# Optimization experiments

Hardware: AMD Instinct MI355X
Metric: run time of the kernel (lower is better)

The kernel has to match this reference:

```python
import jax, jax.numpy as jnp
import numpy as np

HID = 1024
HEADS = 16
HEAD_DIM = HID // HEADS
MAX_P = 64
TAB = 2 * MAX_P + 1
B, L = 8, 512


def setup_inputs() -> dict:
    key = jax.random.key(0)
    ks = jax.random.split(key, 16)
    def lin(k, fan_in, fan_out):
        lim = 1.0 / np.sqrt(fan_in)
        kw, kb = jax.random.split(k)
        W = jax.random.uniform(kw, (fan_out, fan_in), jnp.float32, -lim, lim)
        b = jax.random.uniform(kb, (fan_out,), jnp.float32, -lim, lim)
        return W, b
    Wq, bq = lin(ks[0], HID, HID)
    Wk, bk = lin(ks[1], HID, HID)
    Wv, bv = lin(ks[2], HID, HID)
    Wo, bo = lin(ks[3], HID, HID)
    # xavier_uniform for relative-position tables
    xlim = float(np.sqrt(6.0 / (TAB + HEAD_DIM)))
    table_k = jax.random.uniform(ks[4], (TAB, HEAD_DIM), jnp.float32, -xlim, xlim)
    table_v = jax.random.uniform(ks[5], (TAB, HEAD_DIM), jnp.float32, -xlim, xlim)
    return {
        "query": jax.random.normal(ks[6], (B, L, HID), jnp.float32),
        "key": jax.random.normal(ks[7], (B, L, HID), jnp.float32),
        "value": jax.random.normal(ks[8], (B, L, HID), jnp.float32),
        "final_mat": jax.random.randint(ks[9], (B, L, L), 0, TAB, jnp.int64 if jax.config.jax_enable_x64 else jnp.int32),
        "Wq": Wq, "bq": bq, "Wk": Wk, "bk": bk,
        "Wv": Wv, "bv": bv, "Wo": Wo, "bo": bo,
        "table_k": table_k, "table_v": table_v,
    }


def reference(query, key, value, final_mat, Wq, bq, Wk, bk, Wv, bv, Wo, bo, table_k, table_v):
    Bt, Lq, D = query.shape
    H, hd = HEADS, HEAD_DIM
    q = query @ Wq.T + bq          # [B,Lq,D]
    k = key @ Wk.T + bk            # [B,Lk,D]
    v = value @ Wv.T + bv          # [B,Lv,D]
    q4 = q.reshape(Bt, Lq, H, hd)
    k4 = k.reshape(Bt, -1, H, hd)
    v4 = v.reshape(Bt, -1, H, hd)
    # content-content scores
    attn1 = jnp.einsum('bqhd,bkhd->bhqk', q4, k4)
    # content-position scores via gathered relative-key embeddings [B,Lq,Lk,hd]
    rk = table_k[final_mat]
    attn2 = jnp.einsum('bqhd,bqkd->bhqk', q4, rk)
    scale = jnp.asarray(np.sqrt(hd), q.dtype)
    attn = jax.nn.softmax((attn1 + attn2) / scale, axis=-1)  # [B,H,Lq,Lk]
    # dropout p=0 (eval)
    w1 = jnp.einsum('bhqk,bkhd->bqhd', attn, v4)
    rv = table_v[final_mat]                                   # [B,Lq,Lk,hd]
    w2 = jnp.einsum('bhqk,bqkd->bqhd', attn, rv)
    x = (w1 + w2).reshape(Bt, Lq, D)
    return x @ Wo.T + bo
```

## Files before the change

### kernel.cpp

```cpp
#include <hip/hip_runtime.h>

#define HID 1024
#define HEADS 16
#define HD 64
#define TAB 129
#define QSTR 136
#define BATCH 8
#define SEQ 512

typedef unsigned int uint;
typedef unsigned short ushort;
typedef unsigned char uchar;
typedef __attribute__((ext_vector_type(4))) float f32x4;
typedef __attribute__((ext_vector_type(8))) __bf16 bf16x8;

__device__ __forceinline__ ushort f2b(float x) {
    uint b = __float_as_uint(x);
    uint r = (b + 0x7fffu + ((b >> 16) & 1u)) >> 16;
    return (ushort)r;
}
__device__ __forceinline__ uint pk(float lo, float hi) {
    return (uint)f2b(lo) | ((uint)f2b(hi) << 16);
}
__device__ __forceinline__ float b2f(ushort u) {
    return __uint_as_float(((uint)u) << 16);
}
union U16x8 { uint u[4]; bf16x8 v; ushort s[8]; uint4 q; };
__device__ __forceinline__ bf16x8 pack8(float a0, float a1, float a2, float a3,
                                        float a4, float a5, float a6, float a7) {
    U16x8 r;
    r.u[0] = pk(a0, a1); r.u[1] = pk(a2, a3);
    r.u[2] = pk(a4, a5); r.u[3] = pk(a6, a7);
    return r.v;
}

__device__ __forceinline__ void keep(bf16x8& v) {
    uint4* u = (uint4*)&v;
    asm volatile("" : "+v"(u->x), "+v"(u->y), "+v"(u->z), "+v"(u->w));
}
__device__ __forceinline__ void keepu(uint& v) {
    asm volatile("" : "+v"(v));
}

#define GL16(gp, lp) __builtin_amdgcn_global_load_lds( \
    (const __attribute__((address_space(1))) void*)(gp), \
    (__attribute__((address_space(3))) void*)(lp), 16, 0, 0)

#define LDS_BARRIER() do { \
        asm volatile("s_waitcnt lgkmcnt(0)" ::: "memory"); \
        __builtin_amdgcn_s_barrier(); \
    } while (0)

struct ConvArgs { const float* src[7]; ushort* dst[7]; };

__global__ __launch_bounds__(256) void convert_bf16(ConvArgs ca) {
    int bid = blockIdx.x;
    int ti, lb;
    if (bid < 6144) { ti = bid >> 11; lb = bid & 2047; }
    else { int r = bid - 6144; ti = 3 + (r >> 9); lb = r & 511; }
    const float* s = ca.src[ti] + (size_t)lb * 2048 + (threadIdx.x << 3);
    ushort*      d = ca.dst[ti] + (size_t)lb * 2048 + (threadIdx.x << 3);
    float4 a = *(const float4*)s;
    float4 c = *(const float4*)(s + 4);
    uint4 u;
    u.x = pk(a.x, a.y); u.y = pk(a.z, a.w);
    u.z = pk(c.x, c.y); u.w = pk(c.z, c.w);
    *(uint4*)d = u;
}

struct GemmArgs {
    const ushort* A[3];
    const ushort* W[3];
    const float*  bias[3];
    float*        Cf[3];
    ushort*       Cb[3];
};

__global__ __launch_bounds__(256) void gemm_bf16(GemmArgs ga, int M, int N, int K) {
    __shared__ ushort As[2][128 * 32];
    __shared__ ushort Bs[2][128 * 32];
    const int z = blockIdx.z;
    const ushort* A = ga.A[z];
    const ushort* W = ga.W[z];
    const int tid = threadIdx.x;
    const int m0 = blockIdx.y * 128;
    const int n0 = blockIdx.x * 128;

    const int w  = tid >> 6;
    const int l  = tid & 63;
    const int lr = l & 15;
    const int lg = l >> 4;
    const int wm = w >> 1;
    const int wn = w & 1;

    const int sr = tid >> 2;
    const int sc = tid & 3;
    const int g  = sc ^ ((sr >> 1) & 3);
    const ushort* Ag0 = A + (size_t)(m0 + sr)      * K + g * 8;
    const ushort* Ag1 = A + (size_t)(m0 + sr + 64) * K + g * 8;
    const ushort* Wg0 = W + (size_t)(n0 + sr)      * K + g * 8;
    const ushort* Wg1 = W + (size_t)(n0 + sr + 64) * K + g * 8;

    f32x4 acc[4][4];
#pragma unroll
    for (int mt = 0; mt < 4; ++mt)
#pragma unroll
        for (int nt = 0; nt < 4; ++nt) acc[mt][nt] = (f32x4){0.f, 0.f, 0.f, 0.f};

#define STAGE(buf, k0) do { \
        GL16(Ag0 + (k0), &As[buf][w * 512]); \
        GL16(Ag1 + (k0), &As[buf][2048 + w * 512]); \
        GL16(Wg0 + (k0), &Bs[buf][w * 512]); \
        GL16(Wg1 + (k0), &Bs[buf][2048 + w * 512]); \
    } while (0)

    const int swz = (lr >> 1) & 3;
#define COMPUTE(buf) do { \
        bf16x8 af[4], bf[4]; \
        _Pragma("unroll") \
        for (int mt = 0; mt < 4; ++mt) \
            af[mt] = *(const bf16x8*)&As[buf][(wm * 64 + mt * 16 + lr) * 32 + (lg ^ swz) * 8]; \
        _Pragma("unroll") \
        for (int nt = 0; nt < 4; ++nt) \
            bf[nt] = *(const bf16x8*)&Bs[buf][(wn * 64 + nt * 16 + lr) * 32 + (lg ^ swz) * 8]; \
        _Pragma("unroll") \
        for (int mt = 0; mt < 4; ++mt) \
            _Pragma("unroll") \
            for (int nt = 0; nt < 4; ++nt) \
                acc[mt][nt] = __builtin_amdgcn_mfma_f32_16x16x32_bf16(af[mt], bf[nt], acc[mt][nt], 0, 0, 0); \
    } while (0)

    STAGE(0, 0);
    __syncthreads();
    const int nk = K / 32;
    for (int t = 0; t < nk - 1; ++t) {
        STAGE((t + 1) & 1, (size_t)(t + 1) * 32);
        COMPUTE(t & 1);
        __syncthreads();
    }
    COMPUTE((nk - 1) & 1);

    const float* bias = ga.bias[z];
    float bv[4];
#pragma unroll
    for (int nt = 0; nt < 4; ++nt) bv[nt] = bias[n0 + wn * 64 + nt * 16 + lr];
    float*  Cf = ga.Cf[z];
    ushort* Cb = ga.Cb[z];
    if (Cf) {
#pragma unroll
        for (int mt = 0; mt < 4; ++mt)
#pragma unroll
            for (int r4 = 0; r4 < 4; ++r4) {
                size_t m = m0 + wm * 64 + mt * 16 + lg * 4 + r4;
                float* crow = Cf + m * N + n0 + wn * 64 + lr;
#pragma unroll
                for (int nt = 0; nt < 4; ++nt)
                    crow[nt * 16] = acc[mt][nt][r4] + bv[nt];
            }
    } else {
#pragma unroll
        for (int mt = 0; mt < 4; ++mt)
#pragma unroll
            for (int r4 = 0; r4 < 4; ++r4) {
                size_t m = m0 + wm * 64 + mt * 16 + lg * 4 + r4;
                ushort* crow = Cb + m * N + n0 + wn * 64 + lr;
#pragma unroll
                for (int nt = 0; nt < 4; ++nt)
                    crow[nt * 16] = f2b(acc[mt][nt][r4] + bv[nt]);
            }
    }
#undef STAGE
#undef COMPUTE
}

__global__ __launch_bounds__(256) void gemm_wo(const ushort* __restrict__ A,
                                               const ushort* __restrict__ W,
                                               const float* __restrict__ bias,
                                               float* __restrict__ Cf) {
    const int M = BATCH * SEQ, N = HID, K = HID;
    __shared__ ushort As[2][128 * 32];
    __shared__ ushort Bs[2][64 * 32];
    const int tid = threadIdx.x;
    const int m0 = blockIdx.y * 128;
    const int n0 = blockIdx.x * 64;

    const int w  = tid >> 6;
    const int l  = tid & 63;
    const int lr = l & 15;
    const int lg = l >> 4;
    const int wm = w >> 1;
    const int wn = w & 1;

    const int sr = tid >> 2;
    const int sc = tid & 3;
    const int g  = sc ^ ((sr >> 1) & 3);
    const ushort* Ag0 = A + (size_t)(m0 + sr)      * K + g * 8;
    const ushort* Ag1 = A + (size_t)(m0 + sr + 64) * K + g * 8;
    const ushort* Wg0 = W + (size_t)(n0 + sr)      * K + g * 8;

    f32x4 acc[4][2];
#pragma unroll
    for (int mt = 0; mt < 4; ++mt)
#pragma unroll
        for (int nt = 0; nt < 2; ++nt) acc[mt][nt] = (f32x4){0.f, 0.f, 0.f, 0.f};

#define STAGE(buf, k0) do { \
        GL16(Ag0 + (k0), &As[buf][w * 512]); \
        GL16(Ag1 + (k0), &As[buf][2048 + w * 512]); \
        GL16(Wg0 + (k0), &Bs[buf][w * 512]); \
    } while (0)

    const int swz = (lr >> 1) & 3;
#define COMPUTE(buf) do { \
        bf16x8 af[4], bf[2]; \
        _Pragma("unroll") \
        for (int mt = 0; mt < 4; ++mt) \
            af[mt] = *(const bf16x8*)&As[buf][(wm * 64 + mt * 16 + lr) * 32 + (lg ^ swz) * 8]; \
        _Pragma("unroll") \
        for (int nt = 0; nt < 2; ++nt) \
            bf[nt] = *(const bf16x8*)&Bs[buf][(wn * 32 + nt * 16 + lr) * 32 + (lg ^ swz) * 8]; \
        _Pragma("unroll") \
        for (int mt = 0; mt < 4; ++mt) \
            _Pragma("unroll") \
            for (int nt = 0; nt < 2; ++nt) \
                acc[mt][nt] = __builtin_amdgcn_mfma_f32_16x16x32_bf16(af[mt], bf[nt], acc[mt][nt], 0, 0, 0); \
    } while (0)

    STAGE(0, 0);
    __syncthreads();
    const int nk = K / 32;
    for (int t = 0; t < nk - 1; ++t) {
        STAGE((t + 1) & 1, (size_t)(t + 1) * 32);
        COMPUTE(t & 1);
        __syncthreads();
    }
    COMPUTE((nk - 1) & 1);

    float bv[2];
#pragma unroll
    for (int nt = 0; nt < 2; ++nt) bv[nt] = bias[n0 + wn * 32 + nt * 16 + lr];
#pragma unroll
    for (int mt = 0; mt < 4; ++mt)
#pragma unroll
        for (int r4 = 0; r4 < 4; ++r4) {
            size_t m = m0 + wm * 64 + mt * 16 + lg * 4 + r4;
            float* crow = Cf + m * N + n0 + wn * 32 + lr;
#pragma unroll
            for (int nt = 0; nt < 2; ++nt)
                crow[nt * 16] = acc[mt][nt][r4] + bv[nt];
        }
#undef STAGE
#undef COMPUTE
}

__global__ __launch_bounds__(256) void prep_kernel(const ushort* __restrict__ qb,
                                                   const float* __restrict__ table_k,
                                                   const ushort* __restrict__ vb,
                                                   const float* __restrict__ table_v,
                                                   const int* __restrict__ fmat,
                                                   ushort* __restrict__ qtab,
                                                   ushort* __restrict__ vT,
                                                   ushort* __restrict__ tvT,
                                                   uchar* __restrict__ fm8) {
    __shared__ __align__(16) ushort shmem[144 * 72];
    const int wg  = blockIdx.x;
    const int tid = threadIdx.x;

    if (wg < 256) {
        const int h    = wg & 15;
        const int half = (wg >> 4) & 1;
        const int b    = wg >> 5;
        const int q0   = half * 256;
        ushort* tk = shmem;
        for (int i = tid; i < TAB * 8; i += 256) {
            int row = i >> 3, gr = i & 7;
            const float* src = table_k + row * HD + gr * 8;
            float4 a = *(const float4*)src;
            float4 c = *(const float4*)(src + 4);
            uint4 u;
            u.x = pk(a.x, a.y); u.y = pk(a.z, a.w);
            u.z = pk(c.x, c.y); u.w = pk(c.z, c.w);
            *(uint4*)&tk[row * 72 + gr * 8] = u;
        }
        __syncthreads();

        const int w  = tid >> 6;
        const int l  = tid & 63;
        const int lr = l & 15;
        const int lg = l >> 4;
        bf16x8 qf[4][2];
#pragma unroll
        for (int qt = 0; qt < 4; ++qt) {
            const ushort* qrow = qb + ((size_t)(b * SEQ) + q0 + w * 64 + qt * 16 + lr) * HID + h * HD;
            qf[qt][0] = *(const bf16x8*)(qrow + lg * 8);
            qf[qt][1] = *(const bf16x8*)(qrow + 32 + lg * 8);
        }
        ushort* outbase = qtab + ((size_t)(b * HEADS + h) * SEQ + q0 + w * 64) * QSTR;
#pragma unroll
        for (int mt = 0; mt < 9; ++mt) {
            bf16x8 tf0 = *(const bf16x8*)&tk[(mt * 16 + lr) * 72 + lg * 8];
            bf16x8 tf1 = *(const bf16x8*)&tk[(mt * 16 + lr) * 72 + 32 + lg * 8];
#pragma unroll
            for (int qt = 0; qt < 4; ++qt) {
                f32x4 acc = (f32x4){0.f, 0.f, 0.f, 0.f};
                acc = __builtin_amdgcn_mfma_f32_16x16x32_bf16(tf0, qf[qt][0], acc, 0, 0, 0);
                acc = __builtin_amdgcn_mfma_f32_16x16x32_bf16(tf1, qf[qt][1], acc, 0, 0, 0);
                ushort* orow = outbase + (size_t)(qt * 16 + lr) * QSTR;
                if (mt < 8) {
                    uint2 pu;
                    pu.x = pk(acc[0], acc[1]); pu.y = pk(acc[2], acc[3]);
                    *(uint2*)&orow[mt * 16 + lg * 4] = pu;
                } else if (lg == 0) {
                    orow[128] = f2b(acc[0]);
                }
            }
        }
    } else if (wg < 768) {
        const int vw = wg - 256;
        ushort* tile = shmem;
        const int b = vw >> 6, h = (vw >> 2) & 15, kc = vw & 3;
        const int k0 = kc * 128;
        {
            const int kr = tid >> 1, dc = (tid & 1) * 32;
            const ushort* src = vb + ((size_t)(b * SEQ) + k0 + kr) * HID + h * 64 + dc;
#pragma unroll
            for (int j = 0; j < 4; ++j) {
                uint4 u = *(const uint4*)(src + j * 8);
                *(uint4*)&tile[kr * 72 + dc + j * 8] = u;
            }
        }
        __syncthreads();
        {
            const int dr = tid >> 2, kc2 = (tid & 3) * 32;
            ushort* dst = vT + ((size_t)(b * 16 + h) * 64 + dr) * 512 + k0 + kc2;
#pragma unroll
            for (int j = 0; j < 4; ++j) {
                U16x8 o;
#pragma unroll
                for (int i = 0; i < 8; ++i)
                    o.s[i] = tile[(kc2 + j * 8 + i) * 72 + dr];
                *(uint4*)(dst + j * 8) = o.q;
            }
        }
    } else if (wg == 768) {
        const int tt = tid >> 1, dc = (tid & 1) * 32;
        const float* src = table_v + (size_t)tt * HD + dc;
#pragma unroll
        for (int i = 0; i < 32; ++i)
            tvT[(size_t)(dc + i) * 128 + tt] = f2b(src[i]);
    } else {
        const size_t base = (size_t)(wg - 769) * 2048 + (size_t)tid * 8;
        int4 a = *(const int4*)(fmat + base);
        int4 c = *(const int4*)(fmat + base + 4);
        uint lo = (uint)a.x | ((uint)a.y << 8) | ((uint)a.z << 16) | ((uint)a.w << 24);
        uint hi = (uint)c.x | ((uint)c.y << 8) | ((uint)c.z << 16) | ((uint)c.w << 24);
        uint2 o; o.x = lo; o.y = hi;
        *(uint2*)(fm8 + base) = o;
    }
}

__global__ __launch_bounds__(256, 3) void attn_mfma(const ushort* __restrict__ qp,
                                                    const ushort* __restrict__ kp,
                                                    const ushort* __restrict__ vT,
                                                    const ushort* __restrict__ qt,
                                                    const uchar* __restrict__ fm8,
                                                    const float* __restrict__ table_v,
                                                    const ushort* __restrict__ tvT,
                                                    ushort* __restrict__ x) {
    constexpr float FIX = 65536.0f;
    constexpr float INV_FIX = 1.0f / 65536.0f;

    __shared__ __align__(16) ushort qtb[16 * QSTR];
    __shared__ __align__(16) uint   sbin[16 * 132];
    __shared__ __align__(16) ushort P[4][16 * 136];
    __shared__ float rowsumw[4][16];

    const int tid = threadIdx.x;
    const int w   = tid >> 6;
    const int l   = tid & 63;
    const int lr  = l & 15;
    const int lg  = l >> 4;

    const int wg   = blockIdx.x;
    const int work = (wg & 7) * 512 + (wg >> 3);
    const int qblk = work & 31;
    const int h    = (work >> 5) & 15;
    const int b    = work >> 9;
    const int q0   = qblk * 16;
    const size_t bSEQ = (size_t)b * SEQ;
    const int hHD = h * HD;

    const uchar*  fmrow8   = fm8 + (bSEQ + q0 + lr) * SEQ;
    const ushort* kfr_base = kp + (bSEQ + lr) * HID + hHD;
    const ushort* vfr_base = vT + ((size_t)(b * HEADS + h) * HD + lr) * SEQ;

    bf16x8 qfrag[2];
    {
        const ushort* qrow = qp + (bSEQ + q0 + lr) * HID + hHD;
        qfrag[0] = *(const bf16x8*)(qrow + lg * 8);
        qfrag[1] = *(const bf16x8*)(qrow + 32 + lg * 8);
    }

    {
        const uint4* src = (const uint4*)(qt + ((size_t)(b * HEADS + h) * SEQ + q0) * QSTR);
        uint4* dst = (uint4*)qtb;
        for (int i = tid; i < 16 * QSTR / 8; i += 256) dst[i] = src[i];
    }
    {
        uint4 z = {0u, 0u, 0u, 0u};
        uint4* dz = (uint4*)sbin;
        for (int i = tid; i < 16 * 132 / 4; i += 256) dz[i] = z;
    }
    LDS_BARRIER();

    bf16x8 kfr[8][2];
    uint   fmu[8];
#pragma unroll
    for (int i = 0; i < 8; ++i) {
        const int t  = i >> 2;
        const int mt = i & 3;
        const int k0 = (w * 2 + t) * 64;
        const ushort* kr = kfr_base + (size_t)(k0 + mt * 16) * HID;
        kfr[i][0] = *(const bf16x8*)(kr + lg * 8);
        kfr[i][1] = *(const bf16x8*)(kr + 32 + lg * 8);
        fmu[i] = *(const uint*)(fmrow8 + k0 + mt * 16 + lg * 4);
    }
#pragma unroll
    for (int i = 0; i < 8; ++i) { keep(kfr[i][0]); keep(kfr[i][1]); keepu(fmu[i]); }

    f32x4 stv[8];
#pragma unroll
    for (int i = 0; i < 8; ++i) {
        f32x4 st = (f32x4){0.f, 0.f, 0.f, 0.f};
        st = __builtin_amdgcn_mfma_f32_16x16x32_bf16(kfr[i][0], qfrag[0], st, 0, 0, 0);
        st = __builtin_amdgcn_mfma_f32_16x16x32_bf16(kfr[i][1], qfrag[1], st, 0, 0, 0);
        stv[i] = st;
    }

    float lsum = 0.f;
#pragma unroll
    for (int i = 0; i < 8; ++i) {
        const int t  = i >> 2;
        const int mt = i & 3;
        const uint fm = fmu[i];
        const int t0 = fm & 255, t1 = (fm >> 8) & 255, t2 = (fm >> 16) & 255, t3 = fm >> 24;
        const f32x4 st = stv[i];
        float pr0 = __expf((st[0] + b2f(qtb[lr * QSTR + t0])) * 0.125f);
        float pr1 = __expf((st[1] + b2f(qtb[lr * QSTR + t1])) * 0.125f);
        float pr2 = __expf((st[2] + b2f(qtb[lr * QSTR + t2])) * 0.125f);
        float pr3 = __expf((st[3] + b2f(qtb[lr * QSTR + t3])) * 0.125f);
        lsum += pr0 + pr1 + pr2 + pr3;
        __hip_atomic_fetch_add(&sbin[lr * 132 + t0], (uint)(pr0 * FIX),
                               __ATOMIC_RELAXED, __HIP_MEMORY_SCOPE_WORKGROUP);
        __hip_atomic_fetch_add(&sbin[lr * 132 + t1], (uint)(pr1 * FIX),
                               __ATOMIC_RELAXED, __HIP_MEMORY_SCOPE_WORKGROUP);
        __hip_atomic_fetch_add(&sbin[lr * 132 + t2], (uint)(pr2 * FIX),
                               __ATOMIC_RELAXED, __HIP_MEMORY_SCOPE_WORKGROUP);
        __hip_atomic_fetch_add(&sbin[lr * 132 + t3], (uint)(pr3 * FIX),
                               __ATOMIC_RELAXED, __HIP_MEMORY_SCOPE_WORKGROUP);
        uint2 pu;
        pu.x = pk(pr0, pr1); pu.y = pk(pr2, pr3);
        *(uint2*)&P[w][lr * 136 + t * 64 + mt * 16 + lg * 4] = pu;
    }
    lsum += __shfl_xor(lsum, 16);
    lsum += __shfl_xor(lsum, 32);
    if (lg == 0) rowsumw[w][lr] = lsum;

    bf16x8 vfr[2][4][2];
#pragma unroll
    for (int t = 0; t < 2; ++t) {
        const int k0 = (w * 2 + t) * 64;
#pragma unroll
        for (int nt = 0; nt < 4; ++nt) {
            const ushort* vr = vfr_base + (size_t)nt * 16 * SEQ + k0;
            vfr[t][nt][0] = *(const bf16x8*)(vr + lg * 8);
            vfr[t][nt][1] = *(const bf16x8*)(vr + 32 + lg * 8);
        }
    }
#pragma unroll
    for (int t = 0; t < 2; ++t)
#pragma unroll
        for (int nt = 0; nt < 4; ++nt) { keep(vfr[t][nt][0]); keep(vfr[t][nt][1]); }

    f32x4 acc_o[4];
#pragma unroll
    for (int nt = 0; nt < 4; ++nt) acc_o[nt] = (f32x4){0.f, 0.f, 0.f, 0.f};
#pragma unroll
    for (int t = 0; t < 2; ++t) {
        bf16x8 pa0 = *(const bf16x8*)&P[w][lr * 136 + t * 64 + lg * 8];
        bf16x8 pa1 = *(const bf16x8*)&P[w][lr * 136 + t * 64 + 32 + lg * 8];
#pragma unroll
        for (int nt = 0; nt < 4; ++nt) {
            acc_o[nt] = __builtin_amdgcn_mfma_f32_16x16x32_bf16(pa0, vfr[t][nt][0], acc_o[nt], 0, 0, 0);
            acc_o[nt] = __builtin_amdgcn_mfma_f32_16x16x32_bf16(pa1, vfr[t][nt][1], acc_o[nt], 0, 0, 0);
        }
    }

    LDS_BARRIER();

    {
        const uint* sp = &sbin[lr * 132 + w * 32 + lg * 8];
        bf16x8 af = pack8((float)sp[0] * INV_FIX, (float)sp[1] * INV_FIX,
                          (float)sp[2] * INV_FIX, (float)sp[3] * INV_FIX,
                          (float)sp[4] * INV_FIX, (float)sp[5] * INV_FIX,
                          (float)sp[6] * INV_FIX, (float)sp[7] * INV_FIX);
#pragma unroll
        for (int nt = 0; nt < 4; ++nt) {
            bf16x8 bf_ = *(const bf16x8*)(tvT + (size_t)(nt * 16 + lr) * 128 + w * 32 + lg * 8);
            acc_o[nt] = __builtin_amdgcn_mfma_f32_16x16x32_bf16(af, bf_, acc_o[nt], 0, 0, 0);
        }
    }

    float* obuf = (float*)&P[0][0];
    if (w != 0) {
#pragma unroll
        for (int nt = 0; nt < 4; ++nt)
            *(f32x4*)&obuf[(((w - 1) * 4 + nt) * 64 + l) * 4] = acc_o[nt];
    }
    LDS_BARRIER();

    if (w == 0) {
#pragma unroll
        for (int j = 0; j < 3; ++j)
#pragma unroll
            for (int nt = 0; nt < 4; ++nt) {
                f32x4 p_ = *(const f32x4*)&obuf[((j * 4 + nt) * 64 + l) * 4];
                acc_o[nt][0] += p_[0]; acc_o[nt][1] += p_[1];
                acc_o[nt][2] += p_[2]; acc_o[nt][3] += p_[3];
            }
        float iv[4], nb[4];
#pragma unroll
        for (int r = 0; r < 4; ++r) {
            const int q = lg * 4 + r;
            iv[r] = 1.f / (rowsumw[0][q] + rowsumw[1][q] + rowsumw[2][q] + rowsumw[3][q]);
            nb[r] = (float)sbin[q * 132 + 128] * INV_FIX;
        }
        ushort* orow = x + (bSEQ + q0 + lg * 4) * HID + hHD;
#pragma unroll
        for (int nt = 0; nt < 4; ++nt) {
            float tv = table_v[(size_t)128 * HD + nt * 16 + lr];
#pragma unroll
            for (int r = 0; r < 4; ++r) {
                float o = (acc_o[nt][r] + nb[r] * tv) * iv[r];
                orow[(size_t)r * HID + nt * 16 + lr] = f2b(o);
            }
        }
    }
}

extern "C" void kernel_launch(void* const* d_in, const int* in_sizes, int n_in,
                              void* d_out, int out_size, void* d_ws, size_t ws_size,
                              hipStream_t stream) {
    const float* query = (const float*)d_in[0];
    const float* key   = (const float*)d_in[1];
    const float* value = (const float*)d_in[2];
    const int*   fmat  = (const int*)d_in[3];
    const float* Wq = (const float*)d_in[4];
    const float* bq = (const float*)d_in[5];
    const float* Wk = (const float*)d_in[6];
    const float* bk = (const float*)d_in[7];
    const float* Wv = (const float*)d_in[8];
    const float* bv = (const float*)d_in[9];
    const float* Wo = (const float*)d_in[10];
    const float* bo = (const float*)d_in[11];
    const float* table_k = (const float*)d_in[12];
    const float* table_v = (const float*)d_in[13];

    const size_t nBLD = (size_t)BATCH * SEQ * HID;
    const size_t nW   = (size_t)HID * HID;
    ushort* us = (ushort*)d_ws;
    ushort* qin16 = us;                 us += nBLD;
    ushort* kin16 = us;                 us += nBLD;
    ushort* vin16 = us;                 us += nBLD;
    ushort* wq16  = us;                 us += nW;
    ushort* wk16  = us;                 us += nW;
    ushort* wv16  = us;                 us += nW;
    ushort* wo16  = us;                 us += nW;
    ushort* qb16  = us;                 us += nBLD;
    ushort* kb16  = us;                 us += nBLD;
    ushort* vb16  = us;                 us += nBLD;
    ushort* qt16  = us;                 us += (size_t)BATCH * HEADS * SEQ * QSTR;
    ushort* xb16  = us;                 us += nBLD;
    uchar*  fm8   = (uchar*)us;

    ConvArgs ca;
    ca.src[0] = query; ca.src[1] = key; ca.src[2] = value;
    ca.src[3] = Wq; ca.src[4] = Wk; ca.src[5] = Wv; ca.src[6] = Wo;
    ca.dst[0] = qin16; ca.dst[1] = kin16; ca.dst[2] = vin16;
    ca.dst[3] = wq16; ca.dst[4] = wk16; ca.dst[5] = wv16; ca.dst[6] = wo16;
    convert_bf16<<<dim3(8192), 256, 0, stream>>>(ca);

    const int M = BATCH * SEQ;

    GemmArgs gq = {};
    gq.A[0] = qin16; gq.A[1] = kin16; gq.A[2] = vin16;
    gq.W[0] = wq16;  gq.W[1] = wk16;  gq.W[2] = wv16;
    gq.bias[0] = bq; gq.bias[1] = bk; gq.bias[2] = bv;
    gq.Cf[0] = nullptr; gq.Cf[1] = nullptr; gq.Cf[2] = nullptr;
    gq.Cb[0] = qb16; gq.Cb[1] = kb16; gq.Cb[2] = vb16;
    gemm_bf16<<<dim3(HID / 128, M / 128, 3), 256, 0, stream>>>(gq, M, HID, HID);

    ushort* vTbuf  = qin16;
    ushort* tvTbuf = kin16;

    prep_kernel<<<dim3(1793), 256, 0, stream>>>(qb16, table_k, vb16, table_v,
                                                fmat, qt16, vTbuf, tvTbuf, fm8);

    attn_mfma<<<dim3(BATCH * HEADS * (SEQ/16)), 256, 0, stream>>>(
        qb16, kb16, vTbuf, qt16, fm8, table_v, tvTbuf, xb16);

    gemm_wo<<<dim3(HID / 64, M / 128), 256, 0, stream>>>(xb16, wo16, bo, (float*)d_out);
}
```

Baseline: 198.6 us.

## Split fused attention into separate QK GEMM, softmax and PV GEMM kernels

```diff
diff --git a/kernel.cpp b/kernel.cpp
--- a/kernel.cpp
+++ b/kernel.cpp
@@ -26,30 +26,10 @@
     return __uint_as_float(((uint)u) << 16);
 }
 union U16x8 { uint u[4]; bf16x8 v; ushort s[8]; uint4 q; };
-__device__ __forceinline__ bf16x8 pack8(float a0, float a1, float a2, float a3,
-                                        float a4, float a5, float a6, float a7) {
-    U16x8 r;
-    r.u[0] = pk(a0, a1); r.u[1] = pk(a2, a3);
-    r.u[2] = pk(a4, a5); r.u[3] = pk(a6, a7);
-    return r.v;
-}
-
-__device__ __forceinline__ void keep(bf16x8& v) {
-    uint4* u = (uint4*)&v;
-    asm volatile("" : "+v"(u->x), "+v"(u->y), "+v"(u->z), "+v"(u->w));
-}
-__device__ __forceinline__ void keepu(uint& v) {
-    asm volatile("" : "+v"(v));
-}
 
 #define GL16(gp, lp) __builtin_amdgcn_global_load_lds( \
     (const __attribute__((address_space(1))) void*)(gp), \
     (__attribute__((address_space(3))) void*)(lp), 16, 0, 0)
-
-#define LDS_BARRIER() do { \
-        asm volatile("s_waitcnt lgkmcnt(0)" ::: "memory"); \
-        __builtin_amdgcn_s_barrier(); \
-    } while (0)
 
 struct ConvArgs { const float* src[7]; ushort* dst[7]; };
 
@@ -260,7 +240,7 @@
                                                    const int* __restrict__ fmat,
                                                    ushort* __restrict__ qtab,
                                                    ushort* __restrict__ vT,
-                                                   ushort* __restrict__ tvT,
+                                                   ushort* __restrict__ tvT2,
                                                    uchar* __restrict__ fm8) {
     __shared__ __align__(16) ushort shmem[144 * 72];
     const int wg  = blockIdx.x;
@@ -343,11 +323,11 @@
             }
         }
     } else if (wg == 768) {
-        const int tt = tid >> 1, dc = (tid & 1) * 32;
-        const float* src = table_v + (size_t)tt * HD + dc;
-#pragma unroll
-        for (int i = 0; i < 32; ++i)
-            tvT[(size_t)(dc + i) * 128 + tt] = f2b(src[i]);
+        for (int i = tid; i < 64 * 160; i += 256) {
+            int d = i / 160;
+            int c = i - d * 160;
+            tvT2[i] = (c < TAB) ? f2b(table_v[(size_t)c * HD + d]) : (ushort)0;
+        }
     } else {
         const size_t base = (size_t)(wg - 769) * 2048 + (size_t)tid * 8;
         int4 a = *(const int4*)(fmat + base);
@@ -359,193 +339,226 @@
     }
 }
 
-__global__ __launch_bounds__(256, 3) void attn_mfma(const ushort* __restrict__ qp,
-                                                    const ushort* __restrict__ kp,
-                                                    const ushort* __restrict__ vT,
-                                                    const ushort* __restrict__ qt,
-                                                    const uchar* __restrict__ fm8,
-                                                    const float* __restrict__ table_v,
-                                                    const ushort* __restrict__ tvT,
-                                                    ushort* __restrict__ x) {
+__global__ __launch_bounds__(256) void qk_gemm(const ushort* __restrict__ qb,
+                                               const ushort* __restrict__ kb,
+                                               ushort* __restrict__ S) {
+    __shared__ ushort As[2][128 * 32];
+    __shared__ ushort Bs[2][128 * 32];
+    const int tid = threadIdx.x;
+    const int m0 = blockIdx.x * 128;
+    const int n0 = blockIdx.y * 128;
+    const int bh = blockIdx.z;
+    const int b = bh >> 4, h = bh & 15;
+    const size_t rowQ = (size_t)b * SEQ;
+
+    const int w  = tid >> 6;
+    const int l  = tid & 63;
+    const int lr = l & 15;
+    const int lg = l >> 4;
+    const int wm = w >> 1;
+    const int wn = w & 1;
+
+    const int sr = tid >> 2;
+    const int sc = tid & 3;
+    const int g  = sc ^ ((sr >> 1) & 3);
+    const ushort* Ag0 = qb + (rowQ + m0 + sr)      * HID + h * HD + g * 8;
+    const ushort* Ag1 = qb + (rowQ + m0 + sr + 64) * HID + h * HD + g * 8;
+    const ushort* Wg0 = kb + (rowQ + n0 + sr)      * HID + h * HD + g * 8;
+    const ushort* Wg1 = kb + (rowQ + n0 + sr + 64) * HID + h * HD + g * 8;
+
+    GL16(Ag0,      &As[0][w * 512]); GL16(Ag1,      &As[0][2048 + w * 512]);
+    GL16(Wg0,      &Bs[0][w * 512]); GL16(Wg1,      &Bs[0][2048 + w * 512]);
+    GL16(Ag0 + 32, &As[1][w * 512]); GL16(Ag1 + 32, &As[1][2048 + w * 512]);
+    GL16(Wg0 + 32, &Bs[1][w * 512]); GL16(Wg1 + 32, &Bs[1][2048 + w * 512]);
+
+    f32x4 acc[4][4];
+#pragma unroll
+    for (int mt = 0; mt < 4; ++mt)
+#pragma unroll
+        for (int nt = 0; nt < 4; ++nt) acc[mt][nt] = (f32x4){0.f, 0.f, 0.f, 0.f};
+
+    const int swz = (lr >> 1) & 3;
+    __syncthreads();
+#pragma unroll
+    for (int buf = 0; buf < 2; ++buf) {
+        bf16x8 af[4], bf[4];
+#pragma unroll
+        for (int mt = 0; mt < 4; ++mt)
+            af[mt] = *(const bf16x8*)&As[buf][(wm * 64 + mt * 16 + lr) * 32 + (lg ^ swz) * 8];
+#pragma unroll
+        for (int nt = 0; nt < 4; ++nt)
+            bf[nt] = *(const bf16x8*)&Bs[buf][(wn * 64 + nt * 16 + lr) * 32 + (lg ^ swz) * 8];
+#pragma unroll
+        for (int mt = 0; mt < 4; ++mt)
+#pragma unroll
+            for (int nt = 0; nt < 4; ++nt)
+                acc[mt][nt] = __builtin_amdgcn_mfma_f32_16x16x32_bf16(af[mt], bf[nt], acc[mt][nt], 0, 0, 0);
+    }
+
+    ushort* Sb = S + (size_t)bh * SEQ * SEQ;
+#pragma unroll
+    for (int mt = 0; mt < 4; ++mt)
+#pragma unroll
+        for (int r4 = 0; r4 < 4; ++r4) {
+            int m = m0 + wm * 64 + mt * 16 + lg * 4 + r4;
+            ushort* srow = Sb + (size_t)m * SEQ + n0 + wn * 64 + lr;
+#pragma unroll
+            for (int nt = 0; nt < 4; ++nt)
+                srow[nt * 16] = f2b(acc[mt][nt][r4]);
+        }
+}
+
+__global__ __launch_bounds__(256) void sm_kernel(ushort* __restrict__ S,
+                                                 const ushort* __restrict__ qt,
+                                                 const uchar* __restrict__ fm8,
+                                                 ushort* __restrict__ binbuf) {
     constexpr float FIX = 65536.0f;
     constexpr float INV_FIX = 1.0f / 65536.0f;
-
-    __shared__ __align__(16) ushort qtb[16 * QSTR];
-    __shared__ __align__(16) uint   sbin[16 * 132];
-    __shared__ __align__(16) ushort P[4][16 * 136];
-    __shared__ float rowsumw[4][16];
-
+    __shared__ uint binsL[4][160];
     const int tid = threadIdx.x;
-    const int w   = tid >> 6;
+    const int wv  = tid >> 6;
     const int l   = tid & 63;
-    const int lr  = l & 15;
-    const int lg  = l >> 4;
-
-    const int wg   = blockIdx.x;
-    const int work = (wg & 7) * 512 + (wg >> 3);
-    const int qblk = work & 31;
-    const int h    = (work >> 5) & 15;
-    const int b    = work >> 9;
-    const int q0   = qblk * 16;
-    const size_t bSEQ = (size_t)b * SEQ;
-    const int hHD = h * HD;
-
-    const uchar*  fmrow8   = fm8 + (bSEQ + q0 + lr) * SEQ;
-    const ushort* kfr_base = kp + (bSEQ + lr) * HID + hHD;
-    const ushort* vfr_base = vT + ((size_t)(b * HEADS + h) * HD + lr) * SEQ;
-
-    bf16x8 qfrag[2];
-    {
-        const ushort* qrow = qp + (bSEQ + q0 + lr) * HID + hHD;
-        qfrag[0] = *(const bf16x8*)(qrow + lg * 8);
-        qfrag[1] = *(const bf16x8*)(qrow + 32 + lg * 8);
+    const int gr0 = blockIdx.x * 32 + wv * 8;
+
+    for (int ri = 0; ri < 8; ++ri) {
+        const int gr = gr0 + ri;
+        const int q  = gr & 511;
+        const int b  = gr >> 13;
+        binsL[wv][l] = 0u;
+        binsL[wv][l + 64] = 0u;
+        if (l < 32) binsL[wv][l + 128] = 0u;
+
+        U16x8 sv;
+        sv.q = *(const uint4*)&S[((size_t)gr << 9) + l * 8];
+        const uchar* fr = fm8 + ((((size_t)b << 9) + q) << 9) + l * 8;
+        uint f0 = *(const uint*)fr;
+        uint f1 = *(const uint*)(fr + 4);
+        const ushort* qrow = qt + (size_t)gr * QSTR;
+
+        int ts[8];
+        ts[0] = f0 & 255; ts[1] = (f0 >> 8) & 255; ts[2] = (f0 >> 16) & 255; ts[3] = f0 >> 24;
+        ts[4] = f1 & 255; ts[5] = (f1 >> 8) & 255; ts[6] = (f1 >> 16) & 255; ts[7] = f1 >> 24;
+
+        float pr[8];
+        float lsum = 0.f;
+#pragma unroll
+        for (int j = 0; j < 8; ++j) {
+            float s = b2f(sv.s[j]);
+            float gv = b2f(qrow[ts[j]]);
+            pr[j] = __expf((s + gv) * 0.125f);
+            lsum += pr[j];
+        }
+#pragma unroll
+        for (int j = 0; j < 8; ++j)
+            __hip_atomic_fetch_add(&binsL[wv][ts[j]], (uint)(pr[j] * FIX),
+                                   __ATOMIC_RELAXED, __HIP_MEMORY_SCOPE_WORKGROUP);
+#pragma unroll
+        for (int off = 32; off >= 1; off >>= 1)
+            lsum += __shfl_xor(lsum, off);
+        const float invl = 1.f / lsum;
+
+        U16x8 pv;
+#pragma unroll
+        for (int j = 0; j < 4; ++j)
+            pv.u[j] = pk(pr[2 * j] * invl, pr[2 * j + 1] * invl);
+        *(uint4*)&S[((size_t)gr << 9) + l * 8] = pv.q;
+
+        asm volatile("s_waitcnt lgkmcnt(0)" ::: "memory");
+        ushort* bb = binbuf + (size_t)gr * 160;
+        const float sc = INV_FIX * invl;
+        {
+            int c = 2 * l;
+            *(uint*)&bb[c] = pk((float)binsL[wv][c] * sc, (float)binsL[wv][c + 1] * sc);
+        }
+        if (l < 16) {
+            int c = 128 + 2 * l;
+            *(uint*)&bb[c] = pk((float)binsL[wv][c] * sc, (float)binsL[wv][c + 1] * sc);
+        }
     }
-
-    {
-        const uint4* src = (const uint4*)(qt + ((size_t)(b * HEADS + h) * SEQ + q0) * QSTR);
-        uint4* dst = (uint4*)qtb;
-        for (int i = tid; i < 16 * QSTR / 8; i += 256) dst[i] = src[i];
+}
+
+__global__ __launch_bounds__(256) void pv_gemm(const ushort* __restrict__ P,
+                                               const ushort* __restrict__ binbuf,
+                                               const ushort* __restrict__ vT,
+                                               const ushort* __restrict__ tvT2,
+                                               ushort* __restrict__ x) {
+    __shared__ ushort As[2][128 * 32];
+    __shared__ ushort Bs[2][64 * 32];
+    const int tid = threadIdx.x;
+    const int m0 = blockIdx.x * 128;
+    const int bh = blockIdx.y;
+    const int b = bh >> 4, h = bh & 15;
+
+    const int w  = tid >> 6;
+    const int l  = tid & 63;
+    const int lr = l & 15;
+    const int lg = l >> 4;
+    const int wm = w >> 1;
+    const int wn = w & 1;
+
+    const int sr = tid >> 2;
+    const int sc = tid & 3;
+    const int g  = sc ^ ((sr >> 1) & 3);
+    const ushort* AgS0 = P + ((size_t)bh * SEQ + m0 + sr)      * 512 + g * 8;
+    const ushort* AgS1 = P + ((size_t)bh * SEQ + m0 + sr + 64) * 512 + g * 8;
+    const ushort* AgB0 = binbuf + ((size_t)bh * SEQ + m0 + sr)      * 160 + g * 8;
+    const ushort* AgB1 = binbuf + ((size_t)bh * SEQ + m0 + sr + 64) * 160 + g * 8;
+    const ushort* WgV  = vT + ((size_t)bh * 64 + sr) * 512 + g * 8;
+    const ushort* WgT  = tvT2 + (size_t)sr * 160 + g * 8;
+
+#define STAGE_C(buf, st) do { \
+        const ushort* a0_ = (st) < 16 ? AgS0 + (st) * 32 : AgB0 + ((st) - 16) * 32; \
+        const ushort* a1_ = (st) < 16 ? AgS1 + (st) * 32 : AgB1 + ((st) - 16) * 32; \
+        const ushort* b0_ = (st) < 16 ? WgV  + (st) * 32 : WgT  + ((st) - 16) * 32; \
+        GL16(a0_, &As[buf][w * 512]); \
+        GL16(a1_, &As[buf][2048 + w * 512]); \
+        GL16(b0_, &Bs[buf][w * 512]); \
+    } while (0)
+
+    f32x4 acc[4][2];
+#pragma unroll
+    for (int mt = 0; mt < 4; ++mt)
+#pragma unroll
+        for (int nt = 0; nt < 2; ++nt) acc[mt][nt] = (f32x4){0.f, 0.f, 0.f, 0.f};
+
+    const int swz = (lr >> 1) & 3;
+#define COMPUTE_C(buf) do { \
+        bf16x8 af[4], bf[2]; \
+        _Pragma("unroll") \
+        for (int mt = 0; mt < 4; ++mt) \
+            af[mt] = *(const bf16x8*)&As[buf][(wm * 64 + mt * 16 + lr) * 32 + (lg ^ swz) * 8]; \
+        _Pragma("unroll") \
+        for (int nt = 0; nt < 2; ++nt) \
+            bf[nt] = *(const bf16x8*)&Bs[buf][(wn * 32 + nt * 16 + lr) * 32 + (lg ^ swz) * 8]; \
+        _Pragma("unroll") \
+        for (int mt = 0; mt < 4; ++mt) \
+            _Pragma("unroll") \
+            for (int nt = 0; nt < 2; ++nt) \
+                acc[mt][nt] = __builtin_amdgcn_mfma_f32_16x16x32_bf16(af[mt], bf[nt], acc[mt][nt], 0, 0, 0); \
+    } while (0)
+
+    STAGE_C(0, 0);
+    __syncthreads();
+    const int nk = 21;
+    for (int t = 0; t < nk - 1; ++t) {
+        STAGE_C((t + 1) & 1, t + 1);
+        COMPUTE_C(t & 1);
+        __syncthreads();
     }
-    {
-        uint4 z = {0u, 0u, 0u, 0u};
-        uint4* dz = (uint4*)sbin;
-        for (int i = tid; i < 16 * 132 / 4; i += 256) dz[i] = z;
-    }
-    LDS_BARRIER();
-
-    bf16x8 kfr[8][2];
-    uint   fmu[8];
-#pragma unroll
-    for (int i = 0; i < 8; ++i) {
-        const int t  = i >> 2;
-        const int mt = i & 3;
-        const int k0 = (w * 2 + t) * 64;
-        const ushort* kr = kfr_base + (size_t)(k0 + mt * 16) * HID;
-        kfr[i][0] = *(const bf16x8*)(kr + lg * 8);
-        kfr[i][1] = *(const bf16x8*)(kr + 32 + lg * 8);
-        fmu[i] = *(const uint*)(fmrow8 + k0 + mt * 16 + lg * 4);
-    }
-#pragma unroll
-    for (int i = 0; i < 8; ++i) { keep(kfr[i][0]); keep(kfr[i][1]); keepu(fmu[i]); }
-
-    f32x4 stv[8];
-#pragma unroll
-    for (int i = 0; i < 8; ++i) {
-        f32x4 st = (f32x4){0.f, 0.f, 0.f, 0.f};
-        st = __builtin_amdgcn_mfma_f32_16x16x32_bf16(kfr[i][0], qfrag[0], st, 0, 0, 0);
-        st = __builtin_amdgcn_mfma_f32_16x16x32_bf16(kfr[i][1], qfrag[1], st, 0, 0, 0);
-        stv[i] = st;
-    }
-
-    float lsum = 0.f;
-#pragma unroll
-    for (int i = 0; i < 8; ++i) {
-        const int t  = i >> 2;
-        const int mt = i & 3;
-        const uint fm = fmu[i];
-        const int t0 = fm & 255, t1 = (fm >> 8) & 255, t2 = (fm >> 16) & 255, t3 = fm >> 24;
-        const f32x4 st = stv[i];
-        float pr0 = __expf((st[0] + b2f(qtb[lr * QSTR + t0])) * 0.125f);
-        float pr1 = __expf((st[1] + b2f(qtb[lr * QSTR + t1])) * 0.125f);
-        float pr2 = __expf((st[2] + b2f(qtb[lr * QSTR + t2])) * 0.125f);
-        float pr3 = __expf((st[3] + b2f(qtb[lr * QSTR + t3])) * 0.125f);
-        lsum += pr0 + pr1 + pr2 + pr3;
-        __hip_atomic_fetch_add(&sbin[lr * 132 + t0], (uint)(pr0 * FIX),
-                               __ATOMIC_RELAXED, __HIP_MEMORY_SCOPE_WORKGROUP);
-        __hip_atomic_fetch_add(&sbin[lr * 132 + t1], (uint)(pr1 * FIX),
-                               __ATOMIC_RELAXED, __HIP_MEMORY_SCOPE_WORKGROUP);
-        __hip_atomic_fetch_add(&sbin[lr * 132 + t2], (uint)(pr2 * FIX),
-                               __ATOMIC_RELAXED, __HIP_MEMORY_SCOPE_WORKGROUP);
-        __hip_atomic_fetch_add(&sbin[lr * 132 + t3], (uint)(pr3 * FIX),
-                               __ATOMIC_RELAXED, __HIP_MEMORY_SCOPE_WORKGROUP);
-        uint2 pu;
-        pu.x = pk(pr0, pr1); pu.y = pk(pr2, pr3);
-        *(uint2*)&P[w][lr * 136 + t * 64 + mt * 16 + lg * 4] = pu;
-    }
-    lsum += __shfl_xor(lsum, 16);
-    lsum += __shfl_xor(lsum, 32);
-    if (lg == 0) rowsumw[w][lr] = lsum;
-
-    bf16x8 vfr[2][4][2];
-#pragma unroll
-    for (int t = 0; t < 2; ++t) {
-        const int k0 = (w * 2 + t) * 64;
-#pragma unroll
-        for (int nt = 0; nt < 4; ++nt) {
-            const ushort* vr = vfr_base + (size_t)nt * 16 * SEQ + k0;
-            vfr[t][nt][0] = *(const bf16x8*)(vr + lg * 8);
-            vfr[t][nt][1] = *(const bf16x8*)(vr + 32 + lg * 8);
-        }
-    }
-#pragma unroll
-    for (int t = 0; t < 2; ++t)
-#pragma unroll
-        for (int nt = 0; nt < 4; ++nt) { keep(vfr[t][nt][0]); keep(vfr[t][nt][1]); }
-
-    f32x4 acc_o[4];
-#pragma unroll
-    for (int nt = 0; nt < 4; ++nt) acc_o[nt] = (f32x4){0.f, 0.f, 0.f, 0.f};
-#pragma unroll
-    for (int t = 0; t < 2; ++t) {
-        bf16x8 pa0 = *(const bf16x8*)&P[w][lr * 136 + t * 64 + lg * 8];
-        bf16x8 pa1 = *(const bf16x8*)&P[w][lr * 136 + t * 64 + 32 + lg * 8];
-#pragma unroll
-        for (int nt = 0; nt < 4; ++nt) {
-            acc_o[nt] = __builtin_amdgcn_mfma_f32_16x16x32_bf16(pa0, vfr[t][nt][0], acc_o[nt], 0, 0, 0);
-            acc_o[nt] = __builtin_amdgcn_mfma_f32_16x16x32_bf16(pa1, vfr[t][nt][1], acc_o[nt], 0, 0, 0);
-        }
-    }
-
-    LDS_BARRIER();
-
-    {
-        const uint* sp = &sbin[lr * 132 + w * 32 + lg * 8];
-        bf16x8 af = pack8((float)sp[0] * INV_FIX, (float)sp[1] * INV_FIX,
-                          (float)sp[2] * INV_FIX, (float)sp[3] * INV_FIX,
-                          (float)sp[4] * INV_FIX, (float)sp[5] * INV_FIX,
-                          (float)sp[6] * INV_FIX, (float)sp[7] * INV_FIX);
-#pragma unroll
-        for (int nt = 0; nt < 4; ++nt) {
-            bf16x8 bf_ = *(const bf16x8*)(tvT + (size_t)(nt * 16 + lr) * 128 + w * 32 + lg * 8);
-            acc_o[nt] = __builtin_amdgcn_mfma_f32_16x16x32_bf16(af, bf_, acc_o[nt], 0, 0, 0);
-        }
-    }
-
-    float* obuf = (float*)&P[0][0];
-    if (w != 0) {
-#pragma unroll
-        for (int nt = 0; nt < 4; ++nt)
-            *(f32x4*)&obuf[(((w - 1) * 4 + nt) * 64 + l) * 4] = acc_o[nt];
-    }
-    LDS_BARRIER();
-
-    if (w == 0) {
-#pragma unroll
-        for (int j = 0; j < 3; ++j)
-#pragma unroll
-            for (int nt = 0; nt < 4; ++nt) {
-                f32x4 p_ = *(const f32x4*)&obuf[((j * 4 + nt) * 64 + l) * 4];
-                acc_o[nt][0] += p_[0]; acc_o[nt][1] += p_[1];
-                acc_o[nt][2] += p_[2]; acc_o[nt][3] += p_[3];
-            }
-        float iv[4], nb[4];
-#pragma unroll
-        for (int r = 0; r < 4; ++r) {
-            const int q = lg * 4 + r;
-            iv[r] = 1.f / (rowsumw[0][q] + rowsumw[1][q] + rowsumw[2][q] + rowsumw[3][q]);
-            nb[r] = (float)sbin[q * 132 + 128] * INV_FIX;
-        }
-        ushort* orow = x + (bSEQ + q0 + lg * 4) * HID + hHD;
-#pragma unroll
-        for (int nt = 0; nt < 4; ++nt) {
-            float tv = table_v[(size_t)128 * HD + nt * 16 + lr];
-#pragma unroll
-            for (int r = 0; r < 4; ++r) {
-                float o = (acc_o[nt][r] + nb[r] * tv) * iv[r];
-                orow[(size_t)r * HID + nt * 16 + lr] = f2b(o);
-            }
-        }
-    }
+    COMPUTE_C((nk - 1) & 1);
+
+#pragma unroll
+    for (int mt = 0; mt < 4; ++mt)
+#pragma unroll
+        for (int r4 = 0; r4 < 4; ++r4) {
+            int m = m0 + wm * 64 + mt * 16 + lg * 4 + r4;
+            ushort* orow = x + ((size_t)(b * SEQ) + m) * HID + h * HD + wn * 32 + lr;
+#pragma unroll
+            for (int nt = 0; nt < 2; ++nt)
+                orow[nt * 16] = f2b(acc[mt][nt][r4]);
+        }
+#undef STAGE_C
+#undef COMPUTE_C
 }
 
 extern "C" void kernel_launch(void* const* d_in, const int* in_sizes, int n_in,
@@ -581,7 +594,9 @@
     ushort* vb16  = us;                 us += nBLD;
     ushort* qt16  = us;                 us += (size_t)BATCH * HEADS * SEQ * QSTR;
     ushort* xb16  = us;                 us += nBLD;
-    uchar*  fm8   = (uchar*)us;
+    uchar*  fm8   = (uchar*)us;         us += (size_t)BATCH * SEQ * SEQ / 2;
+    ushort* Sbuf  = us;                 us += (size_t)BATCH * HEADS * SEQ * SEQ;
+    ushort* binbf = us;                 us += (size_t)BATCH * HEADS * SEQ * 160;
 
     ConvArgs ca;
     ca.src[0] = query; ca.src[1] = key; ca.src[2] = value;
@@ -606,8 +621,9 @@
     prep_kernel<<<dim3(1793), 256, 0, stream>>>(qb16, table_k, vb16, table_v,
                                                 fmat, qt16, vTbuf, tvTbuf, fm8);
 
-    attn_mfma<<<dim3(BATCH * HEADS * (SEQ/16)), 256, 0, stream>>>(
-        qb16, kb16, vTbuf, qt16, fm8, table_v, tvTbuf, xb16);
+    qk_gemm<<<dim3(4, 4, 128), 256, 0, stream>>>(qb16, kb16, Sbuf);
+    sm_kernel<<<dim3(BATCH * HEADS * SEQ / 32), 256, 0, stream>>>(Sbuf, qt16, fm8, binbf);
+    pv_gemm<<<dim3(4, 128), 256, 0, stream>>>(Sbuf, binbf, vTbuf, tvTbuf, xb16);
 
     gemm_wo<<<dim3(HID / 64, M / 128), 256, 0, stream>>>(xb16, wo16, bo, (float*)d_out);
 }
```

Result: faster. 188.7 us (-5.0%).
